# Kernel optimization log

Hardware: AMD Instinct MI355X
Metric: run time of the kernel (lower is better)

Reference implementation:

```python
import jax, jax.numpy as jnp
import numpy as np

GAM1 = 1.0
GAM2 = 1.0
EPS = 0.01


def setup_inputs() -> dict:
    key = jax.random.key(0)
    k1, k2 = jax.random.split(key)
    m, p, k = 262144, 128, 10
    x = jax.random.normal(k1, (m, p), dtype=jnp.float32)
    y = jax.random.randint(k2, (m,), 0, k, dtype=jnp.int32)
    return {"x": x, "y": y, "num_classes": k}


def reference(x, y, num_classes):
    m, p = x.shape
    I = jnp.eye(p, dtype=x.dtype)
    scalar = p / (m * EPS)

    # W = x.T, so W @ W.T == x.T @ x  (p x p Gram)
    cov = x.T @ x
    discrimn_empi = jnp.linalg.slogdet(I + GAM1 * scalar * cov)[1] / 2.0
    discrimn_theo = jnp.linalg.slogdet(I + scalar * cov)[1] / 2.0

    # per-class compress loss: logdet(I + p/(n_j*eps) * W_j W_j^T) * n_j / m
    onehot = jax.nn.one_hot(y, num_classes, dtype=x.dtype)  # [m, k]
    counts = onehot.sum(axis=0)                             # [k]

    def class_cov(col):  # col: [m] 0/1 mask for one class
        return (x * col[:, None]).T @ x  # [p, p]

    covs = jax.lax.map(class_cov, onehot.T)  # [k, p, p], sequential over k classes

    safe_counts = jnp.maximum(counts, 1.0)
    scal = p / (safe_counts * EPS)                              # [k]
    lds = jnp.linalg.slogdet(I[None] + scal[:, None, None] * covs)[1]  # [k]
    compress = jnp.sum(jnp.where(counts > 0, lds * counts / m, 0.0)) / 2.0

    total_loss_empi = GAM2 * (-discrimn_empi) + compress
    return total_loss_empi, discrimn_empi, discrimn_theo, compress
```

## Files before the change

### kernel.cpp

```cpp
#include <hip/hip_runtime.h>

#define K 10
#define P 128
#define EPSV 0.01f
#define GAM1 1.0f
#define GAM2 1.0f
#define CH 512
#define SK 64
#define KS 68
#define SORTCH 2048
#define NTHR 256

typedef __attribute__((ext_vector_type(8))) short bf16x8;
typedef __attribute__((ext_vector_type(4))) short s16x4;
typedef __attribute__((ext_vector_type(4))) float f32x4;

static __device__ __forceinline__ short f2bf(float f) {
    unsigned u = __float_as_uint(f);
    u = (u + 0x7FFFu + ((u >> 16) & 1u)) >> 16;
    return (short)u;
}

static __device__ __forceinline__ float rdlane(float v, int srclane) {
    return __int_as_float(__builtin_amdgcn_readlane(__float_as_int(v), srclane));
}

__global__ void hist_kernel(const int* __restrict__ y, int* __restrict__ blk_counts, int m) {
    __shared__ int h[K];
    int t = threadIdx.x;
    if (t < K) h[t] = 0;
    __syncthreads();
    int base = blockIdx.x * SORTCH;
    int rows = min(SORTCH, m - base);
    for (int i = t; i < rows; i += NTHR) atomicAdd(&h[y[base + i]], 1);
    __syncthreads();
    if (t < K) blk_counts[blockIdx.x * K + t] = h[t];
}

__global__ void scan_kernel(const int* __restrict__ blk_counts, int* __restrict__ blk_offsets,
                            int* __restrict__ counts, int* __restrict__ pstart, int nb) {
    __shared__ int s[K][128];
    __shared__ int sps[K + 1];
    int t = threadIdx.x;
    int own[K];
    if (t < 128) {
        for (int c = 0; c < K; ++c) {
            int v = (t < nb) ? blk_counts[t * K + c] : 0;
            own[c] = v;
            s[c][t] = v;
        }
    }
    __syncthreads();
    for (int off = 1; off < 128; off <<= 1) {
        int tmp[K];
        if (t < 128)
            for (int c = 0; c < K; ++c) tmp[c] = (t >= off) ? s[c][t - off] : 0;
        __syncthreads();
        if (t < 128)
            for (int c = 0; c < K; ++c) s[c][t] += tmp[c];
        __syncthreads();
    }
    if (t == 0) {
        int run = 0;
        for (int c = 0; c < K; ++c) {
            sps[c] = run;
            int tot = s[c][127];
            counts[c] = tot;
            pstart[c] = run;
            run += ((tot + CH - 1) / CH) * CH;
        }
        sps[K] = run;
        pstart[K] = run;
    }
    __syncthreads();
    if (t < nb)
        for (int c = 0; c < K; ++c)
            blk_offsets[t * K + c] = sps[c] + s[c][t] - own[c];
}

__global__ void scatter_kernel(const int* __restrict__ y, const int* __restrict__ blk_offsets,
                               int* __restrict__ perm, int m) {
    __shared__ int cur[K];
    int t = threadIdx.x;
    if (t < K) cur[t] = blk_offsets[blockIdx.x * K + t];
    __syncthreads();
    int base = blockIdx.x * SORTCH;
    int rows = min(SORTCH, m - base);
    for (int i = t; i < rows; i += NTHR) {
        int row = base + i;
        int pos = atomicAdd(&cur[y[row]], 1);
        perm[pos] = row;
    }
}

__global__ __launch_bounds__(NTHR) void gram_kernel(const float* __restrict__ x,
                                                    const int* __restrict__ perm,
                                                    const int* __restrict__ pstart,
                                                    float* __restrict__ grams) {
    __shared__ int pm[CH];
    __shared__ short xsT[P * KS];
    int t = threadIdx.x;
    long base = (long)blockIdx.x * CH;
    int cls = 0;
    for (int c = 1; c < K; ++c)
        if (base >= (long)pstart[c]) cls = c;
    for (int i = t; i < CH; i += NTHR) pm[i] = perm[base + i];

    const int lane = t & 63;
    const int wave = t >> 6;
    const int m16 = lane & 15;
    const int quad = lane >> 4;
    const int wr = wave >> 1;
    const int wc = wave & 1;
    const int c2 = t & 63;
    const int rg = t >> 6;

    f32x4 acc[4][4];
#pragma unroll
    for (int a = 0; a < 4; ++a)
#pragma unroll
        for (int b = 0; b < 4; ++b) acc[a][b] = (f32x4){0.f, 0.f, 0.f, 0.f};

    __syncthreads();

    for (int s = 0; s < CH / SK; ++s) {
        int sb = s * SK;
        float2 v[16];
#pragma unroll
        for (int ii = 0; ii < 16; ++ii) {
            int r = pm[sb + rg * 16 + ii];
            if (r >= 0) v[ii] = ((const float2*)(x + (size_t)r * P))[c2];
            else { v[ii].x = 0.f; v[ii].y = 0.f; }
        }
        __syncthreads();
        short b0[16], b1[16];
#pragma unroll
        for (int ii = 0; ii < 16; ++ii) { b0[ii] = f2bf(v[ii].x); b1[ii] = f2bf(v[ii].y); }
        int col0 = 2 * c2, col1 = 2 * c2 + 1;
#pragma unroll
        for (int q = 0; q < 4; ++q) {
            s16x4 w0 = {b0[q * 4], b0[q * 4 + 1], b0[q * 4 + 2], b0[q * 4 + 3]};
            s16x4 w1 = {b1[q * 4], b1[q * 4 + 1], b1[q * 4 + 2], b1[q * 4 + 3]};
            *(s16x4*)&xsT[col0 * KS + rg * 16 + q * 4] = w0;
            *(s16x4*)&xsT[col1 * KS + rg * 16 + q * 4] = w1;
        }
        __syncthreads();
#pragma unroll
        for (int kk = 0; kk < 2; ++kk) {
            int k0 = kk * 32 + quad * 8;
            bf16x8 af[4], bfr[4];
#pragma unroll
            for (int a = 0; a < 4; ++a) {
                int colA = wr * 64 + a * 16 + m16;
                union { bf16x8 v8; s16x4 h[2]; } u;
                u.h[0] = *(s16x4*)&xsT[colA * KS + k0];
                u.h[1] = *(s16x4*)&xsT[colA * KS + k0 + 4];
                af[a] = u.v8;
            }
#pragma unroll
            for (int b = 0; b < 4; ++b) {
                int colB = wc * 64 + b * 16 + m16;
                union { bf16x8 v8; s16x4 h[2]; } u;
                u.h[0] = *(s16x4*)&xsT[colB * KS + k0];
                u.h[1] = *(s16x4*)&xsT[colB * KS + k0 + 4];
                bfr[b] = u.v8;
            }
#pragma unroll
            for (int a = 0; a < 4; ++a)
#pragma unroll
                for (int b = 0; b < 4; ++b)
                    acc[a][b] = __builtin_amdgcn_mfma_f32_16x16x32_bf16(af[a], bfr[b], acc[a][b], 0, 0, 0);
        }
    }
    float* g = grams + (size_t)cls * P * P;
#pragma unroll
    for (int a = 0; a < 4; ++a)
#pragma unroll
        for (int b = 0; b < 4; ++b)
#pragma unroll
            for (int r = 0; r < 4; ++r) {
                int gi = wr * 64 + a * 16 + quad * 4 + r;
                int gj = wc * 64 + b * 16 + m16;
                if (gi <= gj) atomicAdd(&g[gi * P + gj], acc[a][b][r]);
            }
}

__global__ void sum_kernel(const float* __restrict__ grams, float* __restrict__ gsum) {
    int idx = blockIdx.x * 256 + threadIdx.x;
    float s = 0.f;
#pragma unroll
    for (int c = 0; c < K; ++c) s += grams[c * P * P + idx];
    gsum[idx] = s;
}

__global__ __launch_bounds__(256, 1) void logdet_kernel(const float* __restrict__ grams,
                                                        const float* __restrict__ gsum,
                                                        const int* __restrict__ counts,
                                                        float* __restrict__ logd, int m) {
    __shared__ float A[P * P];
    int t = threadIdx.x, b = blockIdx.x;
    float scale;
    if (b == 0) scale = GAM1 * (float)P / ((float)m * EPSV);
    else if (b == 1) scale = (float)P / ((float)m * EPSV);
    else {
        float cnt = (float)counts[b - 2];
        if (cnt < 1.f) cnt = 1.f;
        scale = (float)P / (cnt * EPSV);
    }
    const float* src = (b < 2) ? gsum : (grams + (size_t)(b - 2) * P * P);
    for (int idx = t; idx < P * P; idx += 256) {
        int i = idx >> 7, c = idx & (P - 1);
        int s2 = (i <= c) ? idx : (c * P + i);
        A[idx] = scale * src[s2] + ((i == c) ? 1.f : 0.f);
    }
    __syncthreads();

    const int lane = t & 63;
    const int wid = t >> 6;
    float lsum = 0.f;

    for (int bs = 0; bs < 4; ++bs) {
        const int j0 = bs * 32;
        if (wid == 0) {
            float a[32];
            if (lane < 32) {
#pragma unroll
                for (int cc = 0; cc < 8; ++cc)
                    *(f32x4*)&a[cc * 4] = *(f32x4*)&A[(j0 + lane) * P + j0 + cc * 4];
            } else {
#pragma unroll
                for (int cc = 0; cc < 32; ++cc) a[cc] = 0.f;
            }
            float myinv = 0.f;
#pragma unroll
            for (int tt = 0; tt < 32; ++tt) {
                float utt = rdlane(a[tt], tt);
                float inv = __builtin_amdgcn_rcpf(utt);
                lsum += __logf(utt);
                if (lane == tt) myinv = inv;
                bool act = (lane < 32) && (lane > tt);
                float lm = act ? a[tt] * inv : 0.f;
                if (act) a[tt] = lm;
#pragma unroll
                for (int k2 = tt + 1; k2 < 32; ++k2) {
                    float utk = rdlane(a[k2], tt);
                    a[k2] -= lm * utk;
                }
            }
            if (lane < 32) A[(j0 + lane) * P + j0 + lane] = myinv;

            if (bs < 3) {
                int nc = P - j0 - 32;
                int c0 = j0 + 32 + lane;
                int c1 = c0 + 64;
                bool v0 = lane < nc;
                bool v1 = lane + 64 < nc;
                int c0a = v0 ? c0 : (j0 + 32);
                int c1a = v1 ? c1 : (j0 + 32);
                float ua[32], ub[32];
#pragma unroll
                for (int j = 0; j < 32; ++j) {
                    ua[j] = A[(j0 + j) * P + c0a];
                    ub[j] = A[(j0 + j) * P + c1a];
                }
#pragma unroll
                for (int j = 0; j < 32; ++j) {
#pragma unroll
                    for (int t2 = 0; t2 < j; ++t2) {
                        float ljt = rdlane(a[t2], j);
                        ua[j] -= ljt * ua[t2];
                        ub[j] -= ljt * ub[t2];
                    }
                }
#pragma unroll
                for (int j = 0; j < 32; ++j) {
                    if (v0) A[(j0 + j) * P + c0] = ua[j];
                    if (v1) A[(j0 + j) * P + c1] = ub[j];
                }
            }
        }
        __syncthreads();

        if (bs < 3) {
            int nc = P - j0 - 32;
            int nt = nc >> 2;
            int ntiles = nt * nt;
            for (int tile = t; tile < ntiles; tile += 256) {
                int ti = tile / nt, tk = tile - ti * nt;
                int i0 = j0 + 32 + ti * 4, k0 = j0 + 32 + tk * 4;
                f32x4 acc0 = {0, 0, 0, 0}, acc1 = {0, 0, 0, 0};
                f32x4 acc2 = {0, 0, 0, 0}, acc3 = {0, 0, 0, 0};
#pragma unroll
                for (int j = 0; j < 32; ++j) {
                    const float* row = &A[(j0 + j) * P];
                    float invd = row[j0 + j];
                    f32x4 ui = *(const f32x4*)&row[i0];
                    f32x4 uk = *(const f32x4*)&row[k0];
                    uk *= invd;
                    acc0 += ui[0] * uk;
                    acc1 += ui[1] * uk;
                    acc2 += ui[2] * uk;
                    acc3 += ui[3] * uk;
                }
                f32x4* r0 = (f32x4*)&A[(i0 + 0) * P + k0];
                f32x4* r1 = (f32x4*)&A[(i0 + 1) * P + k0];
                f32x4* r2 = (f32x4*)&A[(i0 + 2) * P + k0];
                f32x4* r3 = (f32x4*)&A[(i0 + 3) * P + k0];
                *r0 -= acc0; *r1 -= acc1; *r2 -= acc2; *r3 -= acc3;
            }
            __syncthreads();
        }
    }
    if (t == 0) logd[b] = lsum;
}

__global__ void final_kernel(const float* __restrict__ logd, const int* __restrict__ counts,
                             float* __restrict__ out, int m) {
    if (threadIdx.x == 0 && blockIdx.x == 0) {
        float empi = 0.5f * logd[0];
        float theo = 0.5f * logd[1];
        float comp = 0.f;
        for (int c = 0; c < K; ++c) {
            float cnt = (float)counts[c];
            if (cnt > 0.f) comp += logd[2 + c] * cnt / (float)m;
        }
        comp *= 0.5f;
        out[0] = GAM2 * (-empi) + comp;
        out[1] = empi;
        out[2] = theo;
        out[3] = comp;
    }
}

extern "C" void kernel_launch(void* const* d_in, const int* in_sizes, int n_in,
                              void* d_out, int out_size, void* d_ws, size_t ws_size,
                              hipStream_t stream) {
    const float* x = (const float*)d_in[0];
    const int* y = (const int*)d_in[1];
    int m = in_sizes[1];
    int nbs = (m + SORTCH - 1) / SORTCH;
    int nbg = (m + CH - 1) / CH + K;

    char* ws = (char*)d_ws;
    float* grams = (float*)ws;
    float* gsum = (float*)(ws + 655360);
    float* logd = (float*)(ws + 720896);
    int* counts = (int*)(ws + 720960);
    int* pstart = (int*)(ws + 721024);
    int* blk_counts = (int*)(ws + 721152);
    int* blk_offsets = (int*)(ws + 721152 + (size_t)nbs * K * 4);
    int* perm = (int*)(ws + 721152 + 2 * (size_t)nbs * K * 4);

    hipMemsetAsync(ws, 0, 655360, stream);
    hipMemsetAsync(perm, 0xFF, (size_t)nbg * CH * 4, stream);

    hist_kernel<<<nbs, NTHR, 0, stream>>>(y, blk_counts, m);
    scan_kernel<<<1, NTHR, 0, stream>>>(blk_counts, blk_offsets, counts, pstart, nbs);
    scatter_kernel<<<nbs, NTHR, 0, stream>>>(y, blk_offsets, perm, m);
    gram_kernel<<<nbg, NTHR, 0, stream>>>(x, perm, pstart, grams);
    sum_kernel<<<P * P / 256, 256, 0, stream>>>(grams, gsum);
    logdet_kernel<<<K + 2, 256, 0, stream>>>(grams, gsum, counts, logd, m);
    final_kernel<<<1, 1, 0, stream>>>(logd, counts, (float*)d_out, m);
}
```

Before: 299.5 us.

## Double-buffer gram staging and replace atomics with per-block partials plus reduction

The gram kernel now prefetches the next 64-row stage of gathered x into registers while MFMAs run on the current stage, using a double-buffered LDS tile, which also removes one barrier per stage. Instead of atomically adding upper-triangle results into per-class grams, each block writes its full 128x128 partial to workspace. A new reduce kernel sums the partials per class using the pstart boundaries and also produces the total gram. This removes atomic contention but adds about 530 blocks x 64KB of partial writes and reads, roughly 35MB of extra traffic, and it relies on each block holding a single class (padded class boundaries).

```diff
diff --git a/kernel.cpp b/kernel.cpp
--- a/kernel.cpp
+++ b/kernel.cpp
@@ -95,16 +95,11 @@
 
 __global__ __launch_bounds__(NTHR) void gram_kernel(const float* __restrict__ x,
                                                     const int* __restrict__ perm,
-                                                    const int* __restrict__ pstart,
-                                                    float* __restrict__ grams) {
+                                                    float* __restrict__ partials) {
     __shared__ int pm[CH];
-    __shared__ short xsT[P * KS];
+    __shared__ short xsT[2][P * KS];
     int t = threadIdx.x;
-    long base = (long)blockIdx.x * CH;
-    int cls = 0;
-    for (int c = 1; c < K; ++c)
-        if (base >= (long)pstart[c]) cls = c;
-    for (int i = t; i < CH; i += NTHR) pm[i] = perm[base + i];
+    for (int i = t; i < CH; i += NTHR) pm[i] = perm[(size_t)blockIdx.x * CH + i];
 
     const int lane = t & 63;
     const int wave = t >> 6;
@@ -123,16 +118,20 @@
 
     __syncthreads();
 
+    float2 v[16];
+#define LOAD_STAGE(S)                                                          \
+    {                                                                          \
+        int sb = (S)*SK;                                                       \
+        _Pragma("unroll") for (int ii = 0; ii < 16; ++ii) {                    \
+            int r = pm[sb + rg * 16 + ii];                                     \
+            if (r >= 0) v[ii] = ((const float2*)(x + (size_t)r * P))[c2];      \
+            else { v[ii].x = 0.f; v[ii].y = 0.f; }                             \
+        }                                                                      \
+    }
+
+    LOAD_STAGE(0)
     for (int s = 0; s < CH / SK; ++s) {
-        int sb = s * SK;
-        float2 v[16];
-#pragma unroll
-        for (int ii = 0; ii < 16; ++ii) {
-            int r = pm[sb + rg * 16 + ii];
-            if (r >= 0) v[ii] = ((const float2*)(x + (size_t)r * P))[c2];
-            else { v[ii].x = 0.f; v[ii].y = 0.f; }
-        }
-        __syncthreads();
+        const int buf = s & 1;
         short b0[16], b1[16];
 #pragma unroll
         for (int ii = 0; ii < 16; ++ii) { b0[ii] = f2bf(v[ii].x); b1[ii] = f2bf(v[ii].y); }
@@ -141,10 +140,11 @@
         for (int q = 0; q < 4; ++q) {
             s16x4 w0 = {b0[q * 4], b0[q * 4 + 1], b0[q * 4 + 2], b0[q * 4 + 3]};
             s16x4 w1 = {b1[q * 4], b1[q * 4 + 1], b1[q * 4 + 2], b1[q * 4 + 3]};
-            *(s16x4*)&xsT[col0 * KS + rg * 16 + q * 4] = w0;
-            *(s16x4*)&xsT[col1 * KS + rg * 16 + q * 4] = w1;
+            *(s16x4*)&xsT[buf][col0 * KS + rg * 16 + q * 4] = w0;
+            *(s16x4*)&xsT[buf][col1 * KS + rg * 16 + q * 4] = w1;
         }
         __syncthreads();
+        if (s < CH / SK - 1) LOAD_STAGE(s + 1)
 #pragma unroll
         for (int kk = 0; kk < 2; ++kk) {
             int k0 = kk * 32 + quad * 8;
@@ -153,16 +153,16 @@
             for (int a = 0; a < 4; ++a) {
                 int colA = wr * 64 + a * 16 + m16;
                 union { bf16x8 v8; s16x4 h[2]; } u;
-                u.h[0] = *(s16x4*)&xsT[colA * KS + k0];
-                u.h[1] = *(s16x4*)&xsT[colA * KS + k0 + 4];
+                u.h[0] = *(s16x4*)&xsT[buf][colA * KS + k0];
+                u.h[1] = *(s16x4*)&xsT[buf][colA * KS + k0 + 4];
                 af[a] = u.v8;
             }
 #pragma unroll
             for (int b = 0; b < 4; ++b) {
                 int colB = wc * 64 + b * 16 + m16;
                 union { bf16x8 v8; s16x4 h[2]; } u;
-                u.h[0] = *(s16x4*)&xsT[colB * KS + k0];
-                u.h[1] = *(s16x4*)&xsT[colB * KS + k0 + 4];
+                u.h[0] = *(s16x4*)&xsT[buf][colB * KS + k0];
+                u.h[1] = *(s16x4*)&xsT[buf][colB * KS + k0 + 4];
                 bfr[b] = u.v8;
             }
 #pragma unroll
@@ -172,7 +172,8 @@
                     acc[a][b] = __builtin_amdgcn_mfma_f32_16x16x32_bf16(af[a], bfr[b], acc[a][b], 0, 0, 0);
         }
     }
-    float* g = grams + (size_t)cls * P * P;
+#undef LOAD_STAGE
+    float* out = partials + (size_t)blockIdx.x * P * P;
 #pragma unroll
     for (int a = 0; a < 4; ++a)
 #pragma unroll
@@ -181,16 +182,33 @@
             for (int r = 0; r < 4; ++r) {
                 int gi = wr * 64 + a * 16 + quad * 4 + r;
                 int gj = wc * 64 + b * 16 + m16;
-                if (gi <= gj) atomicAdd(&g[gi * P + gj], acc[a][b][r]);
-            }
-}
-
-__global__ void sum_kernel(const float* __restrict__ grams, float* __restrict__ gsum) {
-    int idx = blockIdx.x * 256 + threadIdx.x;
-    float s = 0.f;
-#pragma unroll
-    for (int c = 0; c < K; ++c) s += grams[c * P * P + idx];
-    gsum[idx] = s;
+                out[gi * P + gj] = acc[a][b][r];
+            }
+}
+
+__global__ __launch_bounds__(128) void reduce_kernel(const float* __restrict__ partials,
+                                                     const int* __restrict__ pstart,
+                                                     float* __restrict__ grams,
+                                                     float* __restrict__ gsum, int nbg) {
+    int idx = blockIdx.x * 128 + threadIdx.x;
+    float tot = 0.f;
+    int b = 0;
+#pragma unroll
+    for (int c = 0; c < K; ++c) {
+        int bend = (c == K - 1) ? nbg : (pstart[c + 1] / CH);
+        float s0 = 0.f, s1 = 0.f, s2 = 0.f, s3 = 0.f;
+        for (; b + 3 < bend; b += 4) {
+            s0 += partials[(size_t)(b + 0) * P * P + idx];
+            s1 += partials[(size_t)(b + 1) * P * P + idx];
+            s2 += partials[(size_t)(b + 2) * P * P + idx];
+            s3 += partials[(size_t)(b + 3) * P * P + idx];
+        }
+        for (; b < bend; ++b) s0 += partials[(size_t)b * P * P + idx];
+        float s = (s0 + s1) + (s2 + s3);
+        grams[c * P * P + idx] = s;
+        tot += s;
+    }
+    gsum[idx] = tot;
 }
 
 __global__ __launch_bounds__(256, 1) void logdet_kernel(const float* __restrict__ grams,
@@ -210,8 +228,7 @@
     const float* src = (b < 2) ? gsum : (grams + (size_t)(b - 2) * P * P);
     for (int idx = t; idx < P * P; idx += 256) {
         int i = idx >> 7, c = idx & (P - 1);
-        int s2 = (i <= c) ? idx : (c * P + i);
-        A[idx] = scale * src[s2] + ((i == c) ? 1.f : 0.f);
+        A[idx] = scale * src[idx] + ((i == c) ? 1.f : 0.f);
     }
     __syncthreads();
 
@@ -348,17 +365,17 @@
     int* counts = (int*)(ws + 720960);
     int* pstart = (int*)(ws + 721024);
     int* blk_counts = (int*)(ws + 721152);
-    int* blk_offsets = (int*)(ws + 721152 + (size_t)nbs * K * 4);
-    int* perm = (int*)(ws + 721152 + 2 * (size_t)nbs * K * 4);
-
-    hipMemsetAsync(ws, 0, 655360, stream);
+    int* blk_offsets = (int*)(ws + 726272);
+    int* perm = (int*)(ws + 731392);
+    float* partials = (float*)(ws + 1802240);
+
     hipMemsetAsync(perm, 0xFF, (size_t)nbg * CH * 4, stream);
 
     hist_kernel<<<nbs, NTHR, 0, stream>>>(y, blk_counts, m);
     scan_kernel<<<1, NTHR, 0, stream>>>(blk_counts, blk_offsets, counts, pstart, nbs);
     scatter_kernel<<<nbs, NTHR, 0, stream>>>(y, blk_offsets, perm, m);
-    gram_kernel<<<nbg, NTHR, 0, stream>>>(x, perm, pstart, grams);
-    sum_kernel<<<P * P / 256, 256, 0, stream>>>(grams, gsum);
+    gram_kernel<<<nbg, NTHR, 0, stream>>>(x, perm, partials);
+    reduce_kernel<<<P * P / 128, 128, 0, stream>>>(partials, pstart, grams, gsum, nbg);
     logdet_kernel<<<K + 2, 256, 0, stream>>>(grams, gsum, counts, logd, m);
     final_kernel<<<1, 1, 0, stream>>>(logd, counts, (float*)d_out, m);
 }
```

Result: slower. 326.5 us (+9.0%).
